# Kernel tuning notes

Measured on AMD Instinct MI355X. Metric: run time of the kernel, lower is better.

Reference implementation:

```python
import jax, jax.numpy as jnp
import numpy as np

NUM_PERS = 16
D = 128
N = 4096
EPSILON = 0.1
EPS_NORM = 1e-12  # matches torch F.normalize default eps


def setup_inputs() -> dict:
    key = jax.random.key(0)
    k1, k2 = jax.random.split(key)
    context = jax.random.normal(k1, (N, D), dtype=jnp.float32)
    # xavier_uniform for shape (num_pers, input_size): bound = sqrt(6/(fan_in+fan_out))
    bound = float(np.sqrt(6.0 / (NUM_PERS + D)))
    weight_tensor = jax.random.uniform(k2, (NUM_PERS, D), dtype=jnp.float32,
                                       minval=-bound, maxval=bound)
    return {"context": context, "weight_tensor": weight_tensor}


def reference(context, weight_tensor):
    # context: [N, D]; weight_tensor: [P, D]
    # per-perspective weighted features: [P, N, D]
    context_fc = context[None, :, :] * weight_tensor[:, None, :]
    # L2 normalize along feature dim (torch F.normalize: x / max(||x||, eps))
    norm = jnp.maximum(jnp.linalg.norm(context_fc, axis=-1, keepdims=True), EPS_NORM)
    context_norm = context_fc / norm
    # cosine similarity per perspective, mean over perspectives: [N, N]
    attention = jnp.einsum('pnd,pmd->pnm', context_norm, context_norm).mean(0)
    # epsilon neighbourhood with markoff_value = 0
    mask = (attention > EPSILON).astype(attention.dtype)
    return attention * mask
```

## Files before the change

kernel.cpp:

```cpp
#include <hip/hip_runtime.h>
#include <math.h>

#define N 4096
#define D 128
#define P 16
#define KK 2048
#define NTB 16
#define NBLK (NTB * NTB)
#define LCAPD 15000
#define CAP (1u << 20)
#define WIN 1.5e-3f
#define ZSCALE 256.0f
#define OSCALE (1.0f / 16777216.0f * 16.0f)

typedef _Float16 half_t;
typedef __attribute__((ext_vector_type(8))) _Float16 f16x8;
typedef __attribute__((ext_vector_type(4))) float f32x4;
typedef __attribute__((address_space(1))) const unsigned int* gptr_t;
typedef __attribute__((address_space(3))) unsigned int* lptr_t;

__global__ __launch_bounds__(256) void k_pack(const float* __restrict__ c,
                                              const float* __restrict__ w,
                                              double* __restrict__ rnorm,
                                              half_t* __restrict__ zb,
                                              unsigned* gcnt, unsigned* govf,
                                              int do_init) {
    int n = blockIdx.x, tid = threadIdx.x;
    if (do_init && n == 0 && tid == 0) { *gcnt = 0; *govf = 0; }
    int p = tid >> 4, d0 = (tid & 15) * 8;
    const float* cc = c + (size_t)n * D + d0;
    const float* ww = w + (size_t)p * D + d0;
    float cv[8], wv[8];
    *(float4*)&cv[0] = *(const float4*)&cc[0];
    *(float4*)&cv[4] = *(const float4*)&cc[4];
    *(float4*)&wv[0] = *(const float4*)&ww[0];
    *(float4*)&wv[4] = *(const float4*)&ww[4];
    double s = 0.0;
#pragma unroll
    for (int i = 0; i < 8; ++i) {
        double v = (double)cv[i] * (double)wv[i];
        s += v * v;
    }
#pragma unroll
    for (int o = 1; o < 16; o <<= 1) s += __shfl_xor(s, o, 64);
    double rn = 1.0 / fmax(sqrt(s), 1e-12);
    if ((tid & 15) == 0) rnorm[p * N + n] = rn;
    float rnf = (float)rn;
    f16x8 o8;
#pragma unroll
    for (int i = 0; i < 8; ++i) o8[i] = (half_t)(cv[i] * wv[i] * rnf * ZSCALE);
    *(f16x8*)&zb[(size_t)n * KK + tid * 8] = o8;
}

template <bool FUSED>
__global__ __launch_bounds__(512, 2) void k_gemm(const half_t* __restrict__ zb,
                                                 float* __restrict__ out,
                                                 unsigned* __restrict__ gcnt,
                                                 unsigned* __restrict__ govf,
                                                 unsigned* __restrict__ glist) {
    __shared__ __align__(16) half_t smbuf[2][16384];
    __shared__ unsigned wl3[4];

    int tid = threadIdx.x;
    int lane = tid & 63, wid = tid >> 6;
    int wm = wid >> 2, wn = wid & 3;

    int braw = blockIdx.x;
    int b = (braw & 7) * 32 + (braw >> 3);
    int bi = b >> 4, bj = b & 15;
    int n0 = bi * 256, m0 = bj * 256;

    int rsel = lane & 15, kk_c = lane >> 4;
    int pc8 = (kk_c ^ ((rsel >> 1) & 3)) * 8;

    int srow = tid >> 2;
    int schunk8 = ((tid & 3) ^ ((tid >> 3) & 3)) * 8;

    f32x4 acc[8][4] = {};

    auto STAGE = [&](int p, int kt) {
        int k0 = kt * 32;
        half_t* A = &smbuf[p][0];
        half_t* B = &smbuf[p][8192];
        __builtin_amdgcn_global_load_lds(
            (gptr_t)(zb + (size_t)(n0 + srow) * KK + k0 + schunk8),
            (lptr_t)(A + tid * 8), 16, 0, 0);
        __builtin_amdgcn_global_load_lds(
            (gptr_t)(zb + (size_t)(n0 + 128 + srow) * KK + k0 + schunk8),
            (lptr_t)(A + 4096 + tid * 8), 16, 0, 0);
        __builtin_amdgcn_global_load_lds(
            (gptr_t)(zb + (size_t)(m0 + srow) * KK + k0 + schunk8),
            (lptr_t)(B + tid * 8), 16, 0, 0);
        __builtin_amdgcn_global_load_lds(
            (gptr_t)(zb + (size_t)(m0 + 128 + srow) * KK + k0 + schunk8),
            (lptr_t)(B + 4096 + tid * 8), 16, 0, 0);
    };

    STAGE(0, 0);
    asm volatile("s_waitcnt vmcnt(0)" ::: "memory");
    __builtin_amdgcn_sched_barrier(0);
    __builtin_amdgcn_s_barrier();
    __builtin_amdgcn_sched_barrier(0);

#pragma unroll 2
    for (int kt = 0; kt < 64; ++kt) {
        int p = kt & 1;
        if (kt < 63) {
            STAGE(p ^ 1, kt + 1);
            asm volatile("s_waitcnt vmcnt(4)" ::: "memory");
        } else {
            asm volatile("s_waitcnt vmcnt(0)" ::: "memory");
        }
        __builtin_amdgcn_sched_barrier(0);
        __builtin_amdgcn_s_barrier();
        __builtin_amdgcn_sched_barrier(0);

        const half_t* A = &smbuf[p][0];
        const half_t* B = &smbuf[p][8192];
        f16x8 af[4], bfr[4];
#pragma unroll
        for (int fj = 0; fj < 4; ++fj)
            bfr[fj] = *(const f16x8*)&B[(wn * 64 + fj * 16 + rsel) * 32 + pc8];
#pragma unroll
        for (int fi = 0; fi < 4; ++fi)
            af[fi] = *(const f16x8*)&A[(wm * 128 + fi * 16 + rsel) * 32 + pc8];
        __builtin_amdgcn_s_setprio(1);
#pragma unroll
        for (int fi = 0; fi < 4; ++fi)
#pragma unroll
            for (int fj = 0; fj < 4; ++fj)
                acc[fi][fj] = __builtin_amdgcn_mfma_f32_16x16x32_f16(af[fi], bfr[fj], acc[fi][fj], 0, 0, 0);
        __builtin_amdgcn_s_setprio(0);
#pragma unroll
        for (int fi = 0; fi < 4; ++fi)
            af[fi] = *(const f16x8*)&A[(wm * 128 + 64 + fi * 16 + rsel) * 32 + pc8];
        __builtin_amdgcn_s_setprio(1);
#pragma unroll
        for (int fi = 0; fi < 4; ++fi)
#pragma unroll
            for (int fj = 0; fj < 4; ++fj)
                acc[4 + fi][fj] = __builtin_amdgcn_mfma_f32_16x16x32_f16(af[fi], bfr[fj], acc[4 + fi][fj], 0, 0, 0);
        __builtin_amdgcn_s_setprio(0);

        asm volatile("s_waitcnt lgkmcnt(0)" ::: "memory");
        __builtin_amdgcn_sched_barrier(0);
        __builtin_amdgcn_s_barrier();
        __builtin_amdgcn_sched_barrier(0);
    }

    unsigned* lds_list = (unsigned*)&smbuf[0][0];
    if (FUSED) {
        if (tid == 0) wl3[0] = 0;
        __syncthreads();
    }

    int colD = rsel, rq = kk_c;
#pragma unroll
    for (int fi = 0; fi < 8; ++fi)
#pragma unroll
        for (int fj = 0; fj < 4; ++fj) {
            int rbase = n0 + wm * 128 + fi * 16 + rq * 4;
            int ccol = m0 + wn * 64 + fj * 16 + colD;
#pragma unroll
            for (int q = 0; q < 4; ++q) {
                float a = acc[fi][fj][q] * OSCALE;
                float sv;
                if (FUSED) {
                    bool flg = fabsf(a - 0.1f) < WIN;
                    sv = flg ? a : (a > 0.1f ? a : 0.0f);
                    if (flg) {
                        unsigned pos = atomicAdd(&wl3[0], 1u);
                        if (pos < LCAPD)
                            lds_list[pos] = (unsigned)(rbase + q) | ((unsigned)ccol << 12);
                    }
                } else {
                    sv = a;
                }
                out[(size_t)(rbase + q) * N + ccol] = sv;
            }
        }

    if (FUSED) {
        __syncthreads();
        if (tid == 0) {
            unsigned tot = wl3[0];
            unsigned cnt = tot > LCAPD ? LCAPD : tot;
            wl3[2] = cnt;
            wl3[1] = atomicAdd(gcnt, cnt);
            if (tot > LCAPD) atomicOr(govf, 1u);
        }
        __syncthreads();
        unsigned cnt = wl3[2], base = wl3[1];
        for (unsigned e = tid; e < cnt; e += 512) {
            unsigned gi = base + e;
            if (gi < CAP) glist[gi] = lds_list[e];
            else atomicOr(govf, 1u);
        }
    }
}

__global__ __launch_bounds__(256) void k_fix2(const float* __restrict__ c,
                                              const float* __restrict__ w,
                                              const double* __restrict__ rnorm,
                                              const unsigned* __restrict__ gcnt,
                                              const unsigned* __restrict__ glist,
                                              float* __restrict__ out) {
    __shared__ double w2[D * P];
    for (int e = threadIdx.x; e < P * D; e += 256) {
        int p = e >> 7, d = e & 127;
        double wv = (double)w[p * D + d];
        w2[d * P + p] = wv * wv;
    }
    __syncthreads();

    unsigned count = *gcnt;
    if (count > CAP) count = CAP;
    unsigned stride = gridDim.x * 256;
    for (unsigned e = blockIdx.x * 256 + threadIdx.x; e < count; e += stride) {
        unsigned u = glist[e];
        int n = u & 4095, m = (u >> 12) & 4095;
        const float* cn = c + (size_t)n * D;
        const float* cm = c + (size_t)m * D;
        double acc[P];
#pragma unroll
        for (int p = 0; p < P; ++p) acc[p] = 0.0;
        for (int d0 = 0; d0 < D; d0 += 4) {
            float4 a4 = *(const float4*)&cn[d0];
            float4 b4 = *(const float4*)&cm[d0];
            float av[4] = {a4.x, a4.y, a4.z, a4.w};
            float bv[4] = {b4.x, b4.y, b4.z, b4.w};
#pragma unroll
            for (int q = 0; q < 4; ++q) {
                double pr = (double)av[q] * (double)bv[q];
#pragma unroll
                for (int p = 0; p < P; ++p) acc[p] += pr * w2[(d0 + q) * P + p];
            }
        }
        double t = 0.0;
#pragma unroll
        for (int p = 0; p < P; ++p)
            t += acc[p] * (rnorm[p * N + n] * rnorm[p * N + m]);
        double fin = t * 0.0625;
        float res = (fin > 0.1) ? (float)fin : 0.0f;
        out[(size_t)n * N + m] = res;
        if (u >> 24) out[(size_t)m * N + n] = res;
    }
}

__global__ __launch_bounds__(256) void k_guard(const float* __restrict__ c,
                                               const float* __restrict__ w,
                                               const double* __restrict__ rnorm,
                                               const unsigned* __restrict__ govf,
                                               float* __restrict__ out) {
    if (*govf == 0) return;
    __shared__ double w2[D * P];
    for (int e = threadIdx.x; e < P * D; e += 256) {
        int p = e >> 7, d = e & 127;
        double wv = (double)w[p * D + d];
        w2[d * P + p] = wv * wv;
    }
    __syncthreads();
    size_t stride = (size_t)gridDim.x * 256;
    for (size_t idx = (size_t)blockIdx.x * 256 + threadIdx.x; idx < (size_t)N * N;
         idx += stride) {
        float a = out[idx];
        if (fabsf(a - 0.1f) >= WIN) {
            out[idx] = (a > 0.1f) ? a : 0.0f;
            continue;
        }
        int n = (int)(idx >> 12), m = (int)(idx & (N - 1));
        const float* cn = c + (size_t)n * D;
        const float* cm = c + (size_t)m * D;
        double acc[P];
#pragma unroll
        for (int p = 0; p < P; ++p) acc[p] = 0.0;
        for (int d0 = 0; d0 < D; d0 += 4) {
            float4 a4 = *(const float4*)&cn[d0];
            float4 b4 = *(const float4*)&cm[d0];
            float av[4] = {a4.x, a4.y, a4.z, a4.w};
            float bv[4] = {b4.x, b4.y, b4.z, b4.w};
#pragma unroll
            for (int q = 0; q < 4; ++q) {
                double pr = (double)av[q] * (double)bv[q];
#pragma unroll
                for (int p = 0; p < P; ++p) acc[p] += pr * w2[(d0 + q) * P + p];
            }
        }
        double t = 0.0;
#pragma unroll
        for (int p = 0; p < P; ++p)
            t += acc[p] * (rnorm[p * N + n] * rnorm[p * N + m]);
        double fin = t * 0.0625;
        out[idx] = (fin > 0.1) ? (float)fin : 0.0f;
    }
}

__global__ __launch_bounds__(256) void k_fix_full(const float* __restrict__ c,
                                                  const float* __restrict__ w,
                                                  const double* __restrict__ rnorm,
                                                  float* __restrict__ out) {
    __shared__ double w2[D * P];
    for (int e = threadIdx.x; e < P * D; e += 256) {
        int p = e >> 7, d = e & 127;
        double wv = (double)w[p * D + d];
        w2[d * P + p] = wv * wv;
    }
    __syncthreads();
    size_t stride = (size_t)gridDim.x * 256;
    for (size_t idx = (size_t)blockIdx.x * 256 + threadIdx.x; idx < (size_t)N * N;
         idx += stride) {
        float a = out[idx];
        if (fabsf(a - 0.1f) >= WIN) {
            out[idx] = (a > 0.1f) ? a : 0.0f;
            continue;
        }
        int n = (int)(idx >> 12), m = (int)(idx & (N - 1));
        const float* cn = c + (size_t)n * D;
        const float* cm = c + (size_t)m * D;
        double acc[P];
#pragma unroll
        for (int p = 0; p < P; ++p) acc[p] = 0.0;
        for (int d0 = 0; d0 < D; d0 += 4) {
            float4 a4 = *(const float4*)&cn[d0];
            float4 b4 = *(const float4*)&cm[d0];
            float av[4] = {a4.x, a4.y, a4.z, a4.w};
            float bv[4] = {b4.x, b4.y, b4.z, b4.w};
#pragma unroll
            for (int q = 0; q < 4; ++q) {
                double pr = (double)av[q] * (double)bv[q];
#pragma unroll
                for (int p = 0; p < P; ++p) acc[p] += pr * w2[(d0 + q) * P + p];
            }
        }
        double t = 0.0;
#pragma unroll
        for (int p = 0; p < P; ++p)
            t += acc[p] * (rnorm[p * N + n] * rnorm[p * N + m]);
        double fin = t * 0.0625;
        out[idx] = (fin > 0.1) ? (float)fin : 0.0f;
    }
}

extern "C" void kernel_launch(void* const* d_in, const int* in_sizes, int n_in,
                              void* d_out, int out_size, void* d_ws, size_t ws_size,
                              hipStream_t stream) {
    const float* c = (const float*)d_in[0];
    const float* w = (const float*)d_in[1];
    float* out = (float*)d_out;
    char* ws = (char*)d_ws;

    double* rnorm = (double*)ws;
    size_t off = (size_t)P * N * 8;
    unsigned* gcnt = (unsigned*)(ws + off);
    unsigned* govf = gcnt + 1;
    unsigned* glist = (unsigned*)(ws + off + 128);
    half_t* zb = (half_t*)(ws + off + 128 + (size_t)CAP * 4);
    size_t need = off + 128 + (size_t)CAP * 4 + (size_t)N * KK * 2;

    if (ws_size >= need) {
        k_pack<<<N, 256, 0, stream>>>(c, w, rnorm, zb, gcnt, govf, 1);
        k_gemm<true><<<NBLK, 512, 0, stream>>>(zb, out, gcnt, govf, glist);
        k_fix2<<<1024, 256, 0, stream>>>(c, w, rnorm, gcnt, glist, out);
        k_guard<<<1024, 256, 0, stream>>>(c, w, rnorm, govf, out);
    } else {
        half_t* zb2 = (half_t*)(ws + off);
        k_pack<<<N, 256, 0, stream>>>(c, w, rnorm, zb2, nullptr, nullptr, 0);
        k_gemm<false><<<NBLK, 512, 0, stream>>>(zb2, out, nullptr, nullptr, nullptr);
        k_fix_full<<<4096, 256, 0, stream>>>(c, w, rnorm, out);
    }
}
```

Measured before the change: 118.3 us.

## Exploit symmetry of attention matrix and triple-buffer the GEMM K loop

Launches only upper-triangular 256x256 tiles of the symmetric Gram matrix and writes each off-diagonal result to both (i,j) and its transpose (j,i) as float4 stores. This roughly halves the MFMA work and operand loads. The K loop moves from double to triple LDS buffering, keeping two stages in flight. Near-threshold list entries carry a mirror flag bit so the later refinement can handle the transposed copy. The costs are more LDS per block (which may cut occupancy below two blocks per CU), strided transposed stores, and a larger per-block list capacity.

Measured after the change: 107.9 us. 8.8% less time.

```diff
diff --git a/kernel.cpp b/kernel.cpp
--- a/kernel.cpp
+++ b/kernel.cpp
@@ -6,8 +6,8 @@
 #define P 16
 #define KK 2048
 #define NTB 16
-#define NBLK (NTB * NTB)
-#define LCAPD 15000
+#define NBLK (NTB * (NTB + 1) / 2)
+#define LCAPD 20000
 #define CAP (1u << 20)
 #define WIN 1.5e-3f
 #define ZSCALE 256.0f
@@ -58,7 +58,7 @@
                                                  unsigned* __restrict__ gcnt,
                                                  unsigned* __restrict__ govf,
                                                  unsigned* __restrict__ glist) {
-    __shared__ __align__(16) half_t smbuf[2][16384];
+    __shared__ __align__(16) half_t smbuf[3][16384];
     __shared__ unsigned wl3[4];
 
     int tid = threadIdx.x;
@@ -66,9 +66,12 @@
     int wm = wid >> 2, wn = wid & 3;
 
     int braw = blockIdx.x;
-    int b = (braw & 7) * 32 + (braw >> 3);
-    int bi = b >> 4, bj = b & 15;
-    int n0 = bi * 256, m0 = bj * 256;
+    int b = (braw & 7) * 17 + (braw >> 3);
+    int ti = 0;
+    while (b >= NTB - ti) { b -= NTB - ti; ++ti; }
+    int tj = ti + b;
+    int n0 = ti * 256, m0 = tj * 256;
+    bool mir = (ti != tj);
 
     int rsel = lane & 15, kk_c = lane >> 4;
     int pc8 = (kk_c ^ ((rsel >> 1) & 3)) * 8;
@@ -96,25 +99,7 @@
             (lptr_t)(B + 4096 + tid * 8), 16, 0, 0);
     };
 
-    STAGE(0, 0);
-    asm volatile("s_waitcnt vmcnt(0)" ::: "memory");
-    __builtin_amdgcn_sched_barrier(0);
-    __builtin_amdgcn_s_barrier();
-    __builtin_amdgcn_sched_barrier(0);
-
-#pragma unroll 2
-    for (int kt = 0; kt < 64; ++kt) {
-        int p = kt & 1;
-        if (kt < 63) {
-            STAGE(p ^ 1, kt + 1);
-            asm volatile("s_waitcnt vmcnt(4)" ::: "memory");
-        } else {
-            asm volatile("s_waitcnt vmcnt(0)" ::: "memory");
-        }
-        __builtin_amdgcn_sched_barrier(0);
-        __builtin_amdgcn_s_barrier();
-        __builtin_amdgcn_sched_barrier(0);
-
+    auto COMPUTE = [&](int p) {
         const half_t* A = &smbuf[p][0];
         const half_t* B = &smbuf[p][8192];
         f16x8 af[4], bfr[4];
@@ -141,15 +126,38 @@
             for (int fj = 0; fj < 4; ++fj)
                 acc[4 + fi][fj] = __builtin_amdgcn_mfma_f32_16x16x32_f16(af[fi], bfr[fj], acc[4 + fi][fj], 0, 0, 0);
         __builtin_amdgcn_s_setprio(0);
-
-        asm volatile("s_waitcnt lgkmcnt(0)" ::: "memory");
-        __builtin_amdgcn_sched_barrier(0);
-        __builtin_amdgcn_s_barrier();
-        __builtin_amdgcn_sched_barrier(0);
-    }
+    };
+
+#define VMW(nn) asm volatile("s_waitcnt vmcnt(" #nn ")" ::: "memory");        \
+                __builtin_amdgcn_sched_barrier(0);                            \
+                __builtin_amdgcn_s_barrier();                                 \
+                __builtin_amdgcn_sched_barrier(0);
+#define LGW     asm volatile("s_waitcnt lgkmcnt(0)" ::: "memory");            \
+                __builtin_amdgcn_sched_barrier(0);                            \
+                __builtin_amdgcn_s_barrier();                                 \
+                __builtin_amdgcn_sched_barrier(0);
+
+    STAGE(0, 0);
+    STAGE(1, 1);
+
+#pragma unroll 3
+    for (int kt = 0; kt < 60; ++kt) {
+        STAGE((kt + 2) % 3, kt + 2);
+        VMW(8)
+        COMPUTE(kt % 3);
+        LGW
+    }
+    STAGE(2, 62); VMW(8) COMPUTE(0); LGW
+    STAGE(0, 63); VMW(8) COMPUTE(1); LGW
+    VMW(4) COMPUTE(2); LGW
+    VMW(0) COMPUTE(0);
+
+#undef VMW
+#undef LGW
 
     unsigned* lds_list = (unsigned*)&smbuf[0][0];
     if (FUSED) {
+        __syncthreads();
         if (tid == 0) wl3[0] = 0;
         __syncthreads();
     }
@@ -161,6 +169,7 @@
         for (int fj = 0; fj < 4; ++fj) {
             int rbase = n0 + wm * 128 + fi * 16 + rq * 4;
             int ccol = m0 + wn * 64 + fj * 16 + colD;
+            float4 mv;
 #pragma unroll
             for (int q = 0; q < 4; ++q) {
                 float a = acc[fi][fj][q] * OSCALE;
@@ -170,14 +179,17 @@
                     sv = flg ? a : (a > 0.1f ? a : 0.0f);
                     if (flg) {
                         unsigned pos = atomicAdd(&wl3[0], 1u);
-                        if (pos < LCAPD)
-                            lds_list[pos] = (unsigned)(rbase + q) | ((unsigned)ccol << 12);
+                        unsigned ent = (unsigned)(rbase + q) | ((unsigned)ccol << 12) |
+                                       (mir ? (1u << 24) : 0u);
+                        if (pos < LCAPD) lds_list[pos] = ent;
                     }
                 } else {
                     sv = a;
                 }
                 out[(size_t)(rbase + q) * N + ccol] = sv;
+                ((float*)&mv)[q] = sv;
             }
+            if (mir) *(float4*)&out[(size_t)ccol * N + rbase] = mv;
         }
 
     if (FUSED) {
```

## Pre-swizzle packed operand into panel-tiled layout and restructure GEMM pipeline with K=64 stages

Applied to the files above, without the earlier changes.

The pack kernel now writes the fp16 operand in a per-256-row panel, per-32-K tiled layout with the LDS swizzle baked in, so each GEMM stage load is one fully contiguous 16 KB block. The GEMM uses 64 KB double buffers holding two K-slices per stage and interleaves four quarter-loads with quarter MFMA phases, each separated by barriers. This aims to improve global coalescing and overlap loads with compute. The change also doubles the LDS list capacity and removes the mirrored write in the fixup kernel, which risks missing entries if that kernel relied on symmetry. It adds more barriers per iteration.

Measured after the change: 111.2 us. 1.06x faster.

```diff
diff --git a/kernel.cpp b/kernel.cpp
--- a/kernel.cpp
+++ b/kernel.cpp
@@ -7,7 +7,7 @@
 #define KK 2048
 #define NTB 16
 #define NBLK (NTB * NTB)
-#define LCAPD 15000
+#define LCAPD 30000
 #define CAP (1u << 20)
 #define WIN 1.5e-3f
 #define ZSCALE 256.0f
@@ -18,6 +18,8 @@
 typedef __attribute__((ext_vector_type(4))) float f32x4;
 typedef __attribute__((address_space(1))) const unsigned int* gptr_t;
 typedef __attribute__((address_space(3))) unsigned int* lptr_t;
+
+#define MF(a, b, c) __builtin_amdgcn_mfma_f32_16x16x32_f16(a, b, c, 0, 0, 0)
 
 __global__ __launch_bounds__(256) void k_pack(const float* __restrict__ c,
                                               const float* __restrict__ w,
@@ -49,7 +51,13 @@
     f16x8 o8;
 #pragma unroll
     for (int i = 0; i < 8; ++i) o8[i] = (half_t)(cv[i] * wv[i] * rnf * ZSCALE);
-    *(f16x8*)&zb[(size_t)n * KK + tid * 8] = o8;
+
+    int panel = n >> 8, rowin = n & 255;
+    int k = p * 128 + d0;
+    int k2 = k >> 5;
+    int cch = (k >> 3) & 3;
+    int piece = rowin * 4 + (cch ^ ((rowin >> 1) & 3));
+    *(f16x8*)&zb[((size_t)(panel * 64 + k2) * 1024 + piece) * 8] = o8;
 }
 
 template <bool FUSED>
@@ -58,7 +66,7 @@
                                                  unsigned* __restrict__ gcnt,
                                                  unsigned* __restrict__ govf,
                                                  unsigned* __restrict__ glist) {
-    __shared__ __align__(16) half_t smbuf[2][16384];
+    __shared__ __align__(16) half_t smbuf[2][32768];
     __shared__ unsigned wl3[4];
 
     int tid = threadIdx.x;
@@ -70,97 +78,141 @@
     int bi = b >> 4, bj = b & 15;
     int n0 = bi * 256, m0 = bj * 256;
 
-    int rsel = lane & 15, kk_c = lane >> 4;
-    int pc8 = (kk_c ^ ((rsel >> 1) & 3)) * 8;
-
-    int srow = tid >> 2;
-    int schunk8 = ((tid & 3) ^ ((tid >> 3) & 3)) * 8;
+    int rl = lane & 15, kc = lane >> 4;
 
     f32x4 acc[8][4] = {};
 
-    auto STAGE = [&](int p, int kt) {
-        int k0 = kt * 32;
-        half_t* A = &smbuf[p][0];
-        half_t* B = &smbuf[p][8192];
-        __builtin_amdgcn_global_load_lds(
-            (gptr_t)(zb + (size_t)(n0 + srow) * KK + k0 + schunk8),
-            (lptr_t)(A + tid * 8), 16, 0, 0);
-        __builtin_amdgcn_global_load_lds(
-            (gptr_t)(zb + (size_t)(n0 + 128 + srow) * KK + k0 + schunk8),
-            (lptr_t)(A + 4096 + tid * 8), 16, 0, 0);
-        __builtin_amdgcn_global_load_lds(
-            (gptr_t)(zb + (size_t)(m0 + srow) * KK + k0 + schunk8),
-            (lptr_t)(B + tid * 8), 16, 0, 0);
-        __builtin_amdgcn_global_load_lds(
-            (gptr_t)(zb + (size_t)(m0 + 128 + srow) * KK + k0 + schunk8),
-            (lptr_t)(B + 4096 + tid * 8), 16, 0, 0);
+    auto STAGEH = [&](int bsel, int seg, int pn, int k2) {
+#pragma unroll
+        for (int l = 0; l < 2; ++l) {
+            const half_t* src = zb + ((size_t)(pn * 64 + k2) * 8192
+                                      + (size_t)(wid * 128 + l * 64 + lane) * 8);
+            __builtin_amdgcn_global_load_lds(
+                (gptr_t)src,
+                (lptr_t)(&smbuf[0][0] + bsel * 32768 + seg + (wid * 128 + l * 64) * 8),
+                16, 0, 0);
+        }
     };
-
-    STAGE(0, 0);
-    asm volatile("s_waitcnt vmcnt(0)" ::: "memory");
-    __builtin_amdgcn_sched_barrier(0);
-    __builtin_amdgcn_s_barrier();
-    __builtin_amdgcn_sched_barrier(0);
-
-#pragma unroll 2
-    for (int kt = 0; kt < 64; ++kt) {
-        int p = kt & 1;
-        if (kt < 63) {
-            STAGE(p ^ 1, kt + 1);
-            asm volatile("s_waitcnt vmcnt(4)" ::: "memory");
-        } else {
-            asm volatile("s_waitcnt vmcnt(0)" ::: "memory");
-        }
-        __builtin_amdgcn_sched_barrier(0);
-        __builtin_amdgcn_s_barrier();
-        __builtin_amdgcn_sched_barrier(0);
-
-        const half_t* A = &smbuf[p][0];
-        const half_t* B = &smbuf[p][8192];
-        f16x8 af[4], bfr[4];
-#pragma unroll
-        for (int fj = 0; fj < 4; ++fj)
-            bfr[fj] = *(const f16x8*)&B[(wn * 64 + fj * 16 + rsel) * 32 + pc8];
-#pragma unroll
-        for (int fi = 0; fi < 4; ++fi)
-            af[fi] = *(const f16x8*)&A[(wm * 128 + fi * 16 + rsel) * 32 + pc8];
+    auto LDF = [&](int bsel, int seg, int R) -> f16x8 {
+        int r = R + rl;
+        return *(const f16x8*)&smbuf[0][bsel * 32768 + seg +
+                                       (r * 4 + (kc ^ ((r >> 1) & 3))) * 8];
+    };
+
+#define SYNC  __builtin_amdgcn_sched_barrier(0); __builtin_amdgcn_s_barrier(); \
+              __builtin_amdgcn_sched_barrier(0);
+#define VMC(nn) asm volatile("s_waitcnt vmcnt(" #nn ")" ::: "memory");
+
+    STAGEH(0, 0,     bi, 0);
+    STAGEH(0, 8192,  bj, 0);
+    STAGEH(0, 24576, bj, 1);
+    STAGEH(0, 16384, bi, 1);
+    VMC(4) SYNC
+
+    f16x8 af[8], bf0[4], bf1[4];
+
+    for (int kt = 0; kt < 31; ++kt) {
+        int bs = kt & 1, bn = bs ^ 1;
+        int k2n = (kt + 1) * 2;
+#pragma unroll
+        for (int fi = 0; fi < 8; ++fi) af[fi] = LDF(bs, 0, wm * 128 + fi * 16);
+#pragma unroll
+        for (int j = 0; j < 4; ++j) bf0[j] = LDF(bs, 8192, wn * 64 + j * 16);
+        STAGEH(bn, 0, bi, k2n);
+        VMC(4) SYNC
         __builtin_amdgcn_s_setprio(1);
 #pragma unroll
-        for (int fi = 0; fi < 4; ++fi)
-#pragma unroll
-            for (int fj = 0; fj < 4; ++fj)
-                acc[fi][fj] = __builtin_amdgcn_mfma_f32_16x16x32_f16(af[fi], bfr[fj], acc[fi][fj], 0, 0, 0);
+        for (int fi = 0; fi < 8; ++fi) {
+            acc[fi][0] = MF(af[fi], bf0[0], acc[fi][0]);
+            acc[fi][1] = MF(af[fi], bf0[1], acc[fi][1]);
+        }
         __builtin_amdgcn_s_setprio(0);
-#pragma unroll
-        for (int fi = 0; fi < 4; ++fi)
-            af[fi] = *(const f16x8*)&A[(wm * 128 + 64 + fi * 16 + rsel) * 32 + pc8];
+        SYNC
+#pragma unroll
+        for (int j = 0; j < 4; ++j) bf1[j] = LDF(bs, 24576, wn * 64 + j * 16);
+        STAGEH(bn, 8192, bj, k2n);
+        VMC(4) SYNC
         __builtin_amdgcn_s_setprio(1);
 #pragma unroll
-        for (int fi = 0; fi < 4; ++fi)
-#pragma unroll
-            for (int fj = 0; fj < 4; ++fj)
-                acc[4 + fi][fj] = __builtin_amdgcn_mfma_f32_16x16x32_f16(af[fi], bfr[fj], acc[4 + fi][fj], 0, 0, 0);
+        for (int fi = 0; fi < 8; ++fi) {
+            acc[fi][2] = MF(af[fi], bf0[2], acc[fi][2]);
+            acc[fi][3] = MF(af[fi], bf0[3], acc[fi][3]);
+        }
         __builtin_amdgcn_s_setprio(0);
-
-        asm volatile("s_waitcnt lgkmcnt(0)" ::: "memory");
-        __builtin_amdgcn_sched_barrier(0);
-        __builtin_amdgcn_s_barrier();
-        __builtin_amdgcn_sched_barrier(0);
-    }
+        SYNC
+#pragma unroll
+        for (int fi = 0; fi < 8; ++fi) af[fi] = LDF(bs, 16384, wm * 128 + fi * 16);
+        STAGEH(bn, 24576, bj, k2n + 1);
+        VMC(4) SYNC
+        __builtin_amdgcn_s_setprio(1);
+#pragma unroll
+        for (int fi = 0; fi < 8; ++fi) {
+            acc[fi][0] = MF(af[fi], bf1[0], acc[fi][0]);
+            acc[fi][1] = MF(af[fi], bf1[1], acc[fi][1]);
+        }
+        __builtin_amdgcn_s_setprio(0);
+        SYNC
+        STAGEH(bn, 16384, bi, k2n + 1);
+        VMC(4) SYNC
+        __builtin_amdgcn_s_setprio(1);
+#pragma unroll
+        for (int fi = 0; fi < 8; ++fi) {
+            acc[fi][2] = MF(af[fi], bf1[2], acc[fi][2]);
+            acc[fi][3] = MF(af[fi], bf1[3], acc[fi][3]);
+        }
+        __builtin_amdgcn_s_setprio(0);
+        SYNC
+    }
+    {
+#pragma unroll
+        for (int fi = 0; fi < 8; ++fi) af[fi] = LDF(1, 0, wm * 128 + fi * 16);
+#pragma unroll
+        for (int j = 0; j < 4; ++j) bf0[j] = LDF(1, 8192, wn * 64 + j * 16);
+        VMC(2) SYNC
+#pragma unroll
+        for (int fi = 0; fi < 8; ++fi) {
+            acc[fi][0] = MF(af[fi], bf0[0], acc[fi][0]);
+            acc[fi][1] = MF(af[fi], bf0[1], acc[fi][1]);
+        }
+        SYNC
+#pragma unroll
+        for (int j = 0; j < 4; ++j) bf1[j] = LDF(1, 24576, wn * 64 + j * 16);
+        VMC(0) SYNC
+#pragma unroll
+        for (int fi = 0; fi < 8; ++fi) {
+            acc[fi][2] = MF(af[fi], bf0[2], acc[fi][2]);
+            acc[fi][3] = MF(af[fi], bf0[3], acc[fi][3]);
+        }
+        SYNC
+#pragma unroll
+        for (int fi = 0; fi < 8; ++fi) af[fi] = LDF(1, 16384, wm * 128 + fi * 16);
+#pragma unroll
+        for (int fi = 0; fi < 8; ++fi) {
+            acc[fi][0] = MF(af[fi], bf1[0], acc[fi][0]);
+            acc[fi][1] = MF(af[fi], bf1[1], acc[fi][1]);
+        }
+#pragma unroll
+        for (int fi = 0; fi < 8; ++fi) {
+            acc[fi][2] = MF(af[fi], bf1[2], acc[fi][2]);
+            acc[fi][3] = MF(af[fi], bf1[3], acc[fi][3]);
+        }
+    }
+#undef SYNC
+#undef VMC
 
     unsigned* lds_list = (unsigned*)&smbuf[0][0];
+    __syncthreads();
     if (FUSED) {
         if (tid == 0) wl3[0] = 0;
         __syncthreads();
     }
 
-    int colD = rsel, rq = kk_c;
 #pragma unroll
     for (int fi = 0; fi < 8; ++fi)
 #pragma unroll
         for (int fj = 0; fj < 4; ++fj) {
-            int rbase = n0 + wm * 128 + fi * 16 + rq * 4;
-            int ccol = m0 + wn * 64 + fj * 16 + colD;
+            int rbase = n0 + wm * 128 + fi * 16 + kc * 4;
+            int ccol = m0 + wn * 64 + fj * 16 + rl;
 #pragma unroll
             for (int q = 0; q < 4; ++q) {
                 float a = acc[fi][fj][q] * OSCALE;
@@ -241,9 +293,7 @@
         for (int p = 0; p < P; ++p)
             t += acc[p] * (rnorm[p * N + n] * rnorm[p * N + m]);
         double fin = t * 0.0625;
-        float res = (fin > 0.1) ? (float)fin : 0.0f;
-        out[(size_t)n * N + m] = res;
-        if (u >> 24) out[(size_t)m * N + n] = res;
+        out[(size_t)n * N + m] = (fin > 0.1) ? (float)fin : 0.0f;
     }
 }
 
```

## Pre-tile packed operand layout and triple-buffer GEMM with register-prefetched fragments

Applied to the files above, without the earlier changes.

The pack kernel now writes the fp16 operand in a panel-tiled, pre-swizzled layout, so each GEMM stage load is one contiguous 16-byte-per-lane copy into LDS. The GEMM moves from double to triple LDS buffering. It also ping-pongs two register fragment sets, so LDS reads for the next k-tile are issued before the current tile's MFMAs, aiming to hide LDS latency and barrier stalls. In exchange, LDS per block grows to about 96KB, which may leave room for only one block per CU on this hardware, and fragment register pressure rises. The LDS list capacity is raised, and the fixup path no longer mirrors writes to the transposed position.

Measured after the change: 144.2 us. +21.9%, slower.

```diff
diff --git a/kernel.cpp b/kernel.cpp
--- a/kernel.cpp
+++ b/kernel.cpp
@@ -7,7 +7,7 @@
 #define KK 2048
 #define NTB 16
 #define NBLK (NTB * NTB)
-#define LCAPD 15000
+#define LCAPD 24000
 #define CAP (1u << 20)
 #define WIN 1.5e-3f
 #define ZSCALE 256.0f
@@ -18,6 +18,8 @@
 typedef __attribute__((ext_vector_type(4))) float f32x4;
 typedef __attribute__((address_space(1))) const unsigned int* gptr_t;
 typedef __attribute__((address_space(3))) unsigned int* lptr_t;
+
+#define MF(a, b, c) __builtin_amdgcn_mfma_f32_16x16x32_f16(a, b, c, 0, 0, 0)
 
 __global__ __launch_bounds__(256) void k_pack(const float* __restrict__ c,
                                               const float* __restrict__ w,
@@ -49,7 +51,13 @@
     f16x8 o8;
 #pragma unroll
     for (int i = 0; i < 8; ++i) o8[i] = (half_t)(cv[i] * wv[i] * rnf * ZSCALE);
-    *(f16x8*)&zb[(size_t)n * KK + tid * 8] = o8;
+
+    int panel = n >> 8, rowin = n & 255;
+    int k = p * 128 + d0;
+    int k2 = k >> 5;
+    int cch = (k >> 3) & 3;
+    int piece = rowin * 4 + (cch ^ ((rowin >> 1) & 3));
+    *(f16x8*)&zb[((size_t)(panel * 64 + k2) * 1024 + piece) * 8] = o8;
 }
 
 template <bool FUSED>
@@ -58,7 +66,7 @@
                                                  unsigned* __restrict__ gcnt,
                                                  unsigned* __restrict__ govf,
                                                  unsigned* __restrict__ glist) {
-    __shared__ __align__(16) half_t smbuf[2][16384];
+    __shared__ __align__(16) half_t smbuf[3][16384];
     __shared__ unsigned wl3[4];
 
     int tid = threadIdx.x;
@@ -70,97 +78,98 @@
     int bi = b >> 4, bj = b & 15;
     int n0 = bi * 256, m0 = bj * 256;
 
-    int rsel = lane & 15, kk_c = lane >> 4;
-    int pc8 = (kk_c ^ ((rsel >> 1) & 3)) * 8;
-
-    int srow = tid >> 2;
-    int schunk8 = ((tid & 3) ^ ((tid >> 3) & 3)) * 8;
+    int rl = lane & 15, kc = lane >> 4;
 
     f32x4 acc[8][4] = {};
 
     auto STAGE = [&](int p, int kt) {
-        int k0 = kt * 32;
-        half_t* A = &smbuf[p][0];
-        half_t* B = &smbuf[p][8192];
-        __builtin_amdgcn_global_load_lds(
-            (gptr_t)(zb + (size_t)(n0 + srow) * KK + k0 + schunk8),
-            (lptr_t)(A + tid * 8), 16, 0, 0);
-        __builtin_amdgcn_global_load_lds(
-            (gptr_t)(zb + (size_t)(n0 + 128 + srow) * KK + k0 + schunk8),
-            (lptr_t)(A + 4096 + tid * 8), 16, 0, 0);
-        __builtin_amdgcn_global_load_lds(
-            (gptr_t)(zb + (size_t)(m0 + srow) * KK + k0 + schunk8),
-            (lptr_t)(B + tid * 8), 16, 0, 0);
-        __builtin_amdgcn_global_load_lds(
-            (gptr_t)(zb + (size_t)(m0 + 128 + srow) * KK + k0 + schunk8),
-            (lptr_t)(B + 4096 + tid * 8), 16, 0, 0);
+#pragma unroll
+        for (int l = 0; l < 2; ++l) {
+            const half_t* srcA = zb + ((size_t)(bi * 64 + kt) * 8192
+                                       + (size_t)(wid * 128 + l * 64 + lane) * 8);
+            __builtin_amdgcn_global_load_lds(
+                (gptr_t)srcA, (lptr_t)(&smbuf[p][0] + (wid * 128 + l * 64) * 8), 16, 0, 0);
+        }
+#pragma unroll
+        for (int l = 0; l < 2; ++l) {
+            const half_t* srcB = zb + ((size_t)(bj * 64 + kt) * 8192
+                                       + (size_t)(wid * 128 + l * 64 + lane) * 8);
+            __builtin_amdgcn_global_load_lds(
+                (gptr_t)srcB, (lptr_t)(&smbuf[p][8192] + (wid * 128 + l * 64) * 8), 16, 0, 0);
+        }
     };
 
+#define LOADF(P, AF, BF)                                                        \
+    {                                                                           \
+        const half_t* Ab = &smbuf[P][0];                                        \
+        const half_t* Bb = &smbuf[P][8192];                                     \
+        _Pragma("unroll")                                                       \
+        for (int fi = 0; fi < 8; ++fi) {                                        \
+            int r = wm * 128 + fi * 16 + rl;                                    \
+            AF[fi] = *(const f16x8*)&Ab[(r * 4 + (kc ^ ((r >> 1) & 3))) * 8];   \
+        }                                                                       \
+        _Pragma("unroll")                                                       \
+        for (int fj = 0; fj < 4; ++fj) {                                        \
+            int r = wn * 64 + fj * 16 + rl;                                     \
+            BF[fj] = *(const f16x8*)&Bb[(r * 4 + (kc ^ ((r >> 1) & 3))) * 8];   \
+        }                                                                       \
+    }
+
+#define MFMAS(AF, BF)                                                           \
+    __builtin_amdgcn_s_setprio(1);                                              \
+    _Pragma("unroll")                                                           \
+    for (int fi = 0; fi < 8; ++fi)                                              \
+        _Pragma("unroll")                                                       \
+        for (int fj = 0; fj < 4; ++fj)                                          \
+            acc[fi][fj] = MF(AF[fi], BF[fj], acc[fi][fj]);                      \
+    __builtin_amdgcn_s_setprio(0);
+
+#define VMC(nn) asm volatile("s_waitcnt vmcnt(" #nn ")" ::: "memory");          \
+                __builtin_amdgcn_sched_barrier(0);
+#define LGK0    asm volatile("s_waitcnt lgkmcnt(0)" ::: "memory");              \
+                __builtin_amdgcn_sched_barrier(0);
+#define BAR     __builtin_amdgcn_s_barrier();                                   \
+                __builtin_amdgcn_sched_barrier(0);
+
+    f16x8 afA[8], bfA[4], afB[8], bfB[4];
+
     STAGE(0, 0);
-    asm volatile("s_waitcnt vmcnt(0)" ::: "memory");
-    __builtin_amdgcn_sched_barrier(0);
-    __builtin_amdgcn_s_barrier();
-    __builtin_amdgcn_sched_barrier(0);
-
-#pragma unroll 2
-    for (int kt = 0; kt < 64; ++kt) {
-        int p = kt & 1;
-        if (kt < 63) {
-            STAGE(p ^ 1, kt + 1);
-            asm volatile("s_waitcnt vmcnt(4)" ::: "memory");
-        } else {
-            asm volatile("s_waitcnt vmcnt(0)" ::: "memory");
-        }
-        __builtin_amdgcn_sched_barrier(0);
-        __builtin_amdgcn_s_barrier();
-        __builtin_amdgcn_sched_barrier(0);
-
-        const half_t* A = &smbuf[p][0];
-        const half_t* B = &smbuf[p][8192];
-        f16x8 af[4], bfr[4];
-#pragma unroll
-        for (int fj = 0; fj < 4; ++fj)
-            bfr[fj] = *(const f16x8*)&B[(wn * 64 + fj * 16 + rsel) * 32 + pc8];
-#pragma unroll
-        for (int fi = 0; fi < 4; ++fi)
-            af[fi] = *(const f16x8*)&A[(wm * 128 + fi * 16 + rsel) * 32 + pc8];
-        __builtin_amdgcn_s_setprio(1);
-#pragma unroll
-        for (int fi = 0; fi < 4; ++fi)
-#pragma unroll
-            for (int fj = 0; fj < 4; ++fj)
-                acc[fi][fj] = __builtin_amdgcn_mfma_f32_16x16x32_f16(af[fi], bfr[fj], acc[fi][fj], 0, 0, 0);
-        __builtin_amdgcn_s_setprio(0);
-#pragma unroll
-        for (int fi = 0; fi < 4; ++fi)
-            af[fi] = *(const f16x8*)&A[(wm * 128 + 64 + fi * 16 + rsel) * 32 + pc8];
-        __builtin_amdgcn_s_setprio(1);
-#pragma unroll
-        for (int fi = 0; fi < 4; ++fi)
-#pragma unroll
-            for (int fj = 0; fj < 4; ++fj)
-                acc[4 + fi][fj] = __builtin_amdgcn_mfma_f32_16x16x32_f16(af[fi], bfr[fj], acc[4 + fi][fj], 0, 0, 0);
-        __builtin_amdgcn_s_setprio(0);
-
-        asm volatile("s_waitcnt lgkmcnt(0)" ::: "memory");
-        __builtin_amdgcn_sched_barrier(0);
-        __builtin_amdgcn_s_barrier();
-        __builtin_amdgcn_sched_barrier(0);
-    }
+    STAGE(1, 1);
+    VMC(4) BAR
+    LOADF(0, afA, bfA)
+
+    for (int tt = 0; tt < 32; ++tt) {
+        int t0 = tt * 2, t1 = t0 + 1;
+        if (t0 + 2 < 64) STAGE((t0 + 2) % 3, t0 + 2);
+        if (t0 < 62) { VMC(4) } else { VMC(0) }
+        BAR
+        LOADF((t0 + 1) % 3, afB, bfB)
+        MFMAS(afA, bfA)
+        LGK0 BAR
+        if (t1 + 2 < 64) STAGE((t1 + 2) % 3, t1 + 2);
+        if (t1 < 62) { VMC(4) }
+        BAR
+        if (t1 + 1 < 64) LOADF((t1 + 1) % 3, afA, bfA)
+        MFMAS(afB, bfB)
+        if (t1 < 63) { LGK0 BAR }
+    }
+#undef VMC
+#undef LGK0
+#undef BAR
 
     unsigned* lds_list = (unsigned*)&smbuf[0][0];
+    __syncthreads();
     if (FUSED) {
         if (tid == 0) wl3[0] = 0;
         __syncthreads();
     }
 
-    int colD = rsel, rq = kk_c;
 #pragma unroll
     for (int fi = 0; fi < 8; ++fi)
 #pragma unroll
         for (int fj = 0; fj < 4; ++fj) {
-            int rbase = n0 + wm * 128 + fi * 16 + rq * 4;
-            int ccol = m0 + wn * 64 + fj * 16 + colD;
+            int rbase = n0 + wm * 128 + fi * 16 + kc * 4;
+            int ccol = m0 + wn * 64 + fj * 16 + rl;
 #pragma unroll
             for (int q = 0; q < 4; ++q) {
                 float a = acc[fi][fj][q] * OSCALE;
@@ -241,9 +250,7 @@
         for (int p = 0; p < P; ++p)
             t += acc[p] * (rnorm[p * N + n] * rnorm[p * N + m]);
         double fin = t * 0.0625;
-        float res = (fin > 0.1) ? (float)fin : 0.0f;
-        out[(size_t)n * N + m] = res;
-        if (u >> 24) out[(size_t)m * N + n] = res;
+        out[(size_t)n * N + m] = (fin > 0.1) ? (float)fin : 0.0f;
     }
 }
 
```
